# Kernel optimization log

Hardware: AMD Instinct MI355X
Metric: run time of the kernel (lower is better)

## Reference

```python
import jax, jax.numpy as jnp
import numpy as np

B, N, S, K, D = 16, 4096, 1024, 32, 64
MLP = (64, 64, 128)
EPS = 1e-5  # BatchNorm2d default eps


def setup_inputs() -> dict:
    key = jax.random.key(0)
    ks = jax.random.split(key, 16)
    inp = {
        'xyz': jax.random.normal(ks[0], (B, N, 3), dtype=jnp.float32),
        'normals': jax.random.normal(ks[1], (B, N, 3), dtype=jnp.float32),
        'points': jax.random.normal(ks[2], (B, N, D), dtype=jnp.float32),
        'fps_idx': jax.random.randint(ks[3], (B, S), 0, N),
    }
    last = D
    for i, c in enumerate(MLP):
        inp[f'w{i}'] = jax.random.normal(ks[4 + i], (c, last), dtype=jnp.float32) * (1.0 / np.sqrt(last))
        inp[f'b{i}'] = jnp.zeros((c,), dtype=jnp.float32)
        inp[f'g{i}'] = jnp.ones((c,), dtype=jnp.float32)
        inp[f'bt{i}'] = jnp.zeros((c,), dtype=jnp.float32)
        last = c
    return inp


def _group(points, idx):
    # points: [B,N,C], idx: [B,S,K] -> [B,S,K,C]
    b, s, k = idx.shape
    flat = idx.reshape(b, s * k)
    g = jnp.take_along_axis(points, flat[:, :, None], axis=1)
    return g.reshape(b, s, k, points.shape[-1])


def _forward(xyz, normals, points, fps_idx, params):
    new_xyz = jnp.take_along_axis(xyz, fps_idx[:, :, None], axis=1)        # [B,S,3]
    new_normals = jnp.take_along_axis(normals, fps_idx[:, :, None], axis=1)
    # squared distances [B,S,N] (algebraic form of the broadcasted cdist)
    d = (jnp.sum(new_xyz ** 2, -1)[:, :, None]
         + jnp.sum(xyz ** 2, -1)[:, None, :]
         - 2.0 * jnp.einsum('bsc,bnc->bsn', new_xyz, xyz))
    _, idx = jax.lax.top_k(-d, K)                                          # K nearest
    x = _group(points, idx)                                                # [B,S,K,D]
    x = jnp.transpose(x, (0, 3, 2, 1))                                     # [B,D,K,S]
    for (w, b, g, bt) in params:
        x = jnp.einsum('oc,bcks->boks', w, x) + b[None, :, None, None]     # 1x1 conv
        m = jnp.mean(x, axis=(0, 2, 3), keepdims=True)                     # BN (batch stats)
        v = jnp.var(x, axis=(0, 2, 3), keepdims=True)
        x = (x - m) * jax.lax.rsqrt(v + EPS) * g[None, :, None, None] + bt[None, :, None, None]
        x = jax.nn.relu(x)
    feat = jnp.transpose(jnp.max(x, axis=2), (0, 2, 1))                    # [B,S,C_out]
    return new_xyz, new_normals, feat, fps_idx


def reference(xyz, normals, points, fps_idx,
              w0, b0, g0, bt0, w1, b1, g1, bt1, w2, b2, g2, bt2):
    params = ((w0, b0, g0, bt0), (w1, b1, g1, bt1), (w2, b2, g2, bt2))
    return _forward(xyz, normals, points, fps_idx, params)
```

## Files before the change

kernel.cpp:

```cpp
#include <hip/hip_runtime.h>
#include <hip/hip_bf16.h>

#define B_ 16
#define N_ 4096
#define S_ 1024
#define K_ 32
#define D_ 64
#define M_ (B_*S_*K_)
#define EPS_ 1e-5f

#define OUT_NRM  (B_*S_*3)
#define OUT_FEAT (2*B_*S_*3)
#define OUT_FPS  (OUT_FEAT + B_*S_*128)

typedef __attribute__((ext_vector_type(8))) short bf16x8;
typedef __attribute__((ext_vector_type(4))) float f32x4;
typedef unsigned long long u64;

__device__ __forceinline__ unsigned short rnb(float x){
  return (unsigned short)((__float_as_uint(x) + 0x8000u) >> 16);
}
__device__ __forceinline__ void split1(float x, short& h, short& l){
  unsigned ux = __float_as_uint(x);
  unsigned uh = (ux + 0x8000u) & 0xFFFF0000u;
  h = (short)(uh >> 16);
  float lo = x - __uint_as_float(uh);
  l = (short)((__float_as_uint(lo) + 0x8000u) >> 16);
}
__device__ __forceinline__ unsigned f2key(float d){
  unsigned u = __float_as_uint(d);
  return u ^ ((unsigned)(((int)u) >> 31) | 0x80000000u);
}
__device__ __forceinline__ unsigned mprefix(u64 m){
  return __builtin_amdgcn_mbcnt_hi((unsigned)(m >> 32),
         __builtin_amdgcn_mbcnt_lo((unsigned)m, 0u));
}

__device__ __forceinline__ float hred4_sum(const float v[4], int l){
  bool hi8 = (l & 8) != 0;
  float send0 = hi8 ? v[0] : v[2];
  float send1 = hi8 ? v[1] : v[3];
  float r0 = __shfl_xor(send0, 8);
  float r1 = __shfl_xor(send1, 8);
  float a0 = (hi8 ? v[2] : v[0]) + r0;
  float a1 = (hi8 ? v[3] : v[1]) + r1;
  bool hi4 = (l & 4) != 0;
  float send = hi4 ? a0 : a1;
  float r = __shfl_xor(send, 4);
  float a = (hi4 ? a1 : a0) + r;
  a += __shfl_xor(a, 2);
  a += __shfl_xor(a, 1);
  return a;
}
__device__ __forceinline__ float hred4_max(const float v[4], int l){
  bool hi8 = (l & 8) != 0;
  float send0 = hi8 ? v[0] : v[2];
  float send1 = hi8 ? v[1] : v[3];
  float r0 = __shfl_xor(send0, 8);
  float r1 = __shfl_xor(send1, 8);
  float a0 = fmaxf(hi8 ? v[2] : v[0], r0);
  float a1 = fmaxf(hi8 ? v[3] : v[1], r1);
  bool hi4 = (l & 4) != 0;
  float send = hi4 ? a0 : a1;
  float r = __shfl_xor(send, 4);
  float a = fmaxf(hi4 ? a1 : a0, r);
  a = fmaxf(a, __shfl_xor(a, 2));
  a = fmaxf(a, __shfl_xor(a, 1));
  return a;
}

__device__ __forceinline__ void bsort64_f32x2(float& v0, float& v1, int l){
  #pragma unroll
  for (int k = 2; k <= 64; k <<= 1){
    #pragma unroll
    for (int j = k >> 1; j > 0; j >>= 1){
      bool keepmn = (((l & k) == 0) == ((l & j) == 0));
      float o0 = __shfl_xor(v0, j);
      float o1 = __shfl_xor(v1, j);
      v0 = keepmn ? fminf(v0, o0) : fmaxf(v0, o0);
      v1 = keepmn ? fminf(v1, o1) : fmaxf(v1, o1);
    }
  }
}
__device__ __forceinline__ void bsort64_u64x2(u64& v0, u64& v1, int l){
  #pragma unroll
  for (int k = 2; k <= 64; k <<= 1){
    #pragma unroll
    for (int j = k >> 1; j > 0; j >>= 1){
      bool keepmn = (((l & k) == 0) == ((l & j) == 0));
      u64 o0 = __shfl_xor((unsigned long long)v0, j);
      u64 o1 = __shfl_xor((unsigned long long)v1, j);
      bool a0 = v0 < o0, a1 = v1 < o1;
      v0 = (a0 == keepmn) ? v0 : o0;
      v1 = (a1 == keepmn) ? v1 : o1;
    }
  }
}

__global__ void prep_kernel(const float* __restrict__ xyz, const float* __restrict__ nrm,
                            const int* __restrict__ fps,
                            const float* __restrict__ w0, const float* __restrict__ w1,
                            const float* __restrict__ w2,
                            float* __restrict__ out, float4* __restrict__ px,
                            unsigned short* __restrict__ wdst, float* __restrict__ stats){
  const int bid = blockIdx.x, tid = threadIdx.x;
  if (bid < 256){
    int t = bid*256 + tid;
    const float* p = xyz + (size_t)t*3;
    float x = p[0], y = p[1], z = p[2];
    float pp = __fadd_rn(__fadd_rn(__fmul_rn(x,x), __fmul_rn(y,y)), __fmul_rn(z,z));
    px[t] = make_float4(__fmul_rn(-2.f,x), __fmul_rn(-2.f,y), __fmul_rn(-2.f,z), pp);
  } else if (bid < 320){
    int t = (bid-256)*256 + tid;
    int b = t >> 10;
    int n = fps[t];
    const float* xp = xyz + ((size_t)b*N_ + n)*3;
    out[t*3+0] = xp[0]; out[t*3+1] = xp[1]; out[t*3+2] = xp[2];
    const float* pp = nrm + ((size_t)b*N_ + n)*3;
    out[OUT_NRM + t*3+0] = pp[0]; out[OUT_NRM + t*3+1] = pp[1]; out[OUT_NRM + t*3+2] = pp[2];
    out[OUT_FPS + t] = (float)n;
  } else if (bid < 384){
    int e = (bid-320)*256 + tid;
    const float* W; int base;
    if (e < 4096){ W = w0; base = 0; }
    else if (e < 8192){ W = w1; base = 4096; }
    else { W = w2; base = 8192; }
    int r = e - base;
    int frag = r >> 9;
    int lane = (r >> 3) & 63;
    int j = r & 7;
    int cht = frag >> 1, ks = frag & 1;
    int m = lane & 15, quad = lane >> 4;
    int ch = cht*16 + m, k = ks*32 + quad*8 + j;
    wdst[e] = rnb(W[ch*64 + k]);
  } else {
    stats[(bid-384)*256 + tid] = 0.f;
  }
}

#define DISTA(P,QX,QY,QZ,QQ) __builtin_fmaf((P).x,(QX), \
  __builtin_fmaf((P).y,(QY), __builtin_fmaf((P).z,(QZ), (P).w + (QQ))))

__device__ __forceinline__ float dist_exact(float4 P, float qx, float qy, float qz, float qq){
  float px = -0.5f*P.x, py = -0.5f*P.y, pz = -0.5f*P.z;
  float dt = __fadd_rn(__fadd_rn(__fmul_rn(qx,px), __fmul_rn(qy,py)), __fmul_rn(qz,pz));
  return __fsub_rn(__fadd_rn(qq,P.w), __fmul_rn(2.f,dt));
}

#define MARGIN_ 1e-3f

__device__ __forceinline__ void sel_fallback(const u64* sp, unsigned tot, int l,
                                             int* __restrict__ outp){
  if (tot <= 64){
    u64 pair = sp[l];
    u64 plo = 0, phi = (1ull << 44) - 1;
    for (int it = 0; it < 44; ++it){
      u64 mid = plo + ((phi - plo) >> 1);
      u64 m = __ballot(pair <= mid);
      if (__popcll(m) >= 32) phi = mid; else plo = mid + 1;
    }
    bool sel = (pair <= plo);
    u64 m = __ballot(sel);
    unsigned pos = mprefix(m);
    if (sel) outp[pos] = (int)(pair & 0xFFFull);
  } else {
    u64 pa = sp[l], pb = sp[64 + l];
    u64 plo = 0, phi = (1ull << 44) - 1;
    for (int it = 0; it < 44; ++it){
      u64 mid = plo + ((phi - plo) >> 1);
      int c = __popcll(__ballot(pa <= mid)) + __popcll(__ballot(pb <= mid));
      if (c >= 32) phi = mid; else plo = mid + 1;
    }
    int ca = (pa <= plo) ? 1 : 0;
    int cb = (pb <= plo) ? 1 : 0;
    int c2 = ca + cb, inc = c2;
    #pragma unroll
    for (int off = 1; off < 64; off <<= 1){
      int tv = __shfl_up(inc, off);
      if (l >= off) inc += tv;
    }
    int pos = inc - c2;
    if (ca){ outp[pos] = (int)(pa & 0xFFFull); pos++; }
    if (cb){ outp[pos] = (int)(pb & 0xFFFull); }
  }
}

__global__ __launch_bounds__(256, 8) void knn_kernel(const float4* __restrict__ pxyz,
                                                     const int* __restrict__ fps,
                                                     int* __restrict__ idxout){
  __shared__ u64 spair[4][2][128];
  const int t = threadIdx.x, w = t >> 6, l = t & 63;
  const int b = blockIdx.x >> 7;
  const float4* __restrict__ Pp = pxyz + (size_t)b*N_;
  const int q0 = blockIdx.x*8 + w*2;
  const int nq0 = fps[q0], nq1 = fps[q0+1];
  const float4 Q0 = Pp[nq0], Q1 = Pp[nq1];
  const float qx0 = -0.5f*Q0.x, qy0 = -0.5f*Q0.y, qz0 = -0.5f*Q0.z, qq0 = Q0.w;
  const float qx1 = -0.5f*Q1.x, qy1 = -0.5f*Q1.y, qz1 = -0.5f*Q1.z, qq1 = Q1.w;

  float vmin0 = 3.0e38f, vmin1 = 3.0e38f;
  #pragma unroll 8
  for (int i = 0; i < 64; i++){
    float4 P = Pp[i*64 + l];
    float d0 = DISTA(P, qx0, qy0, qz0, qq0); vmin0 = fminf(vmin0, d0);
    float d1 = DISTA(P, qx1, qy1, qz1, qq1); vmin1 = fminf(vmin1, d1);
  }

  float s0 = vmin0, s1 = vmin1;
  bsort64_f32x2(s0, s1, l);
  const float Tm0 = __shfl(s0, 31) + MARGIN_;
  const float Tm1 = __shfl(s1, 31) + MARGIN_;

  spair[w][0][l] = ~0ull; spair[w][0][64 + l] = ~0ull;
  spair[w][1][l] = ~0ull; spair[w][1][64 + l] = ~0ull;

  unsigned cnt0 = 0, cnt1 = 0;
  #pragma unroll 4
  for (int i = 0; i < 64; i++){
    unsigned n = (unsigned)(i*64 + l);
    float4 P = Pp[n];
    {
      float da = DISTA(P, qx0, qy0, qz0, qq0);
      bool c = (da <= Tm0);
      u64 m = __ballot(c);
      if (c){
        float de = dist_exact(P, qx0, qy0, qz0, qq0);
        unsigned pos = cnt0 + mprefix(m);
        if (pos < 128) spair[w][0][pos] = ((u64)f2key(de) << 12) | n;
      }
      cnt0 += (unsigned)__popcll(m);
    }
    {
      float da = DISTA(P, qx1, qy1, qz1, qq1);
      bool c = (da <= Tm1);
      u64 m = __ballot(c);
      if (c){
        float de = dist_exact(P, qx1, qy1, qz1, qq1);
        unsigned pos = cnt1 + mprefix(m);
        if (pos < 128) spair[w][1][pos] = ((u64)f2key(de) << 12) | n;
      }
      cnt1 += (unsigned)__popcll(m);
    }
  }

  const size_t obase = (size_t)q0 * K_;
  if (cnt0 <= 64 && cnt1 <= 64){
    u64 P0 = spair[w][0][l], P1 = spair[w][1][l];
    bsort64_u64x2(P0, P1, l);
    if (l < 32){
      idxout[obase + l]      = (int)(P0 & 0xFFFull);
      idxout[obase + K_ + l] = (int)(P1 & 0xFFFull);
    }
  } else {
    sel_fallback(&spair[w][0][0], cnt0, l, idxout + obase);
    sel_fallback(&spair[w][1][0], cnt1, l, idxout + obase + K_);
  }
}

__global__ __launch_bounds__(256, 4) void conv1_mfma(const float* __restrict__ pts,
    const int* __restrict__ idx, const unsigned short* __restrict__ wpk,
    const float* __restrict__ bias, unsigned short* __restrict__ Yo,
    float* __restrict__ stats){
  __shared__ float sred[4][128];
  __shared__ uint4 Wl4[512];
  const unsigned short* Wl = (const unsigned short*)Wl4;
  const int t = threadIdx.x, w = t>>6, l = t&63, quad = l>>4, lr = l&15;
  const int m0 = blockIdx.x*128;
  const int Rw = m0 + w*32;
  const int b = m0 >> 15;
  Wl4[t] = ((const uint4*)wpk)[t];
  Wl4[256 + t] = ((const uint4*)wpk)[256 + t];
  f32x4 acc[4][2];
  #pragma unroll
  for (int c = 0; c < 4; c++)
    #pragma unroll
    for (int rt = 0; rt < 2; rt++)
      acc[c][rt] = (f32x4){0.f,0.f,0.f,0.f};
  int ri[2];
  #pragma unroll
  for (int rt = 0; rt < 2; rt++) ri[rt] = idx[Rw + rt*16 + lr];
  __syncthreads();
  #pragma unroll
  for (int s = 0; s < 2; s++){
    bf16x8 wfs[4];
    #pragma unroll
    for (int c = 0; c < 4; c++)
      wfs[c] = *(const bf16x8*)(Wl + (((c*2+s)<<6) + l)*8);
    #pragma unroll
    for (int rt = 0; rt < 2; rt++){
      const float* pr = pts + ((size_t)(b*4096 + ri[rt]))*64;
      float4 v0 = *(const float4*)(pr + s*32 + quad*8);
      float4 v1 = *(const float4*)(pr + s*32 + quad*8 + 4);
      float xs[8] = {v0.x,v0.y,v0.z,v0.w,v1.x,v1.y,v1.z,v1.w};
      bf16x8 xh, xl;
      #pragma unroll
      for (int j = 0; j < 8; j++){ short hh, ll; split1(xs[j], hh, ll); xh[j]=hh; xl[j]=ll; }
      #pragma unroll
      for (int c = 0; c < 4; c++){
        acc[c][rt] = __builtin_amdgcn_mfma_f32_16x16x32_bf16(wfs[c], xh, acc[c][rt], 0,0,0);
        acc[c][rt] = __builtin_amdgcn_mfma_f32_16x16x32_bf16(wfs[c], xl, acc[c][rt], 0,0,0);
      }
    }
  }
  const int rtg0 = Rw >> 4;
  #pragma unroll
  for (int c = 0; c < 4; c++){
    float4 bq = *(const float4*)(bias + c*16 + quad*4);
    float bqa[4] = {bq.x, bq.y, bq.z, bq.w};
    float sv[4] = {0,0,0,0}, qv[4] = {0,0,0,0};
    int kb = c*2 + (quad>>1);
    int sub = (quad&1)*4;
    #pragma unroll
    for (int rt = 0; rt < 2; rt++){
      float y[4];
      #pragma unroll
      for (int r = 0; r < 4; r++){
        y[r] = acc[c][rt][r] + bqa[r];
        sv[r] += y[r];
        qv[r] += y[r]*y[r];
      }
      uint2 p;
      p.x = (unsigned)rnb(y[0]) | ((unsigned)rnb(y[1])<<16);
      p.y = (unsigned)rnb(y[2]) | ((unsigned)rnb(y[3])<<16);
      *(uint2*)(Yo + ((((rtg0+rt)*8 + kb)*16 + lr)*8 + sub)) = p;
    }
    float S = hred4_sum(sv, l);
    float Q = hred4_sum(qv, l);
    if ((l & 3) == 0){
      int ch = c*16 + quad*4 + ((l>>3)&1)*2 + ((l>>2)&1);
      sred[w][ch] = S;
      sred[w][64 + ch] = Q;
    }
  }
  __syncthreads();
  if (t < 128){
    float tot = sred[0][t]+sred[1][t]+sred[2][t]+sred[3][t];
    unsafeAtomicAdd(&stats[(blockIdx.x & 7)*512 + t], tot);
  }
}

__global__ __launch_bounds__(256, 4) void conv2_mfma(const unsigned short* __restrict__ Yi,
    const unsigned short* __restrict__ wpk, const float* __restrict__ bias,
    const float* __restrict__ gg, const float* __restrict__ btv,
    unsigned short* __restrict__ Yo, float* __restrict__ stats){
  __shared__ float sred[4][128];
  __shared__ float sAff[128];
  __shared__ uint4 Wl4[512];
  const unsigned short* Wl = (const unsigned short*)Wl4;
  const int t = threadIdx.x, w = t>>6, l = t&63, quad = l>>4, lr = l&15;
  const int m0 = blockIdx.x*128;
  const int Rw = m0 + w*32;
  Wl4[t] = ((const uint4*)wpk)[t];
  Wl4[256 + t] = ((const uint4*)wpk)[256 + t];
  if (t < 64){
    const float inv = 1.f/(float)M_;
    float S = 0.f, Q = 0.f;
    #pragma unroll
    for (int r = 0; r < 8; r++){
      S += stats[r*512 + t];
      Q += stats[r*512 + 64 + t];
    }
    float mean = S * inv;
    float var  = Q * inv - mean*mean;
    float a = gg[t] * rsqrtf(var + EPS_);
    sAff[t] = a;
    sAff[64 + t] = btv[t] - mean*a;
  }
  f32x4 acc[4][2];
  #pragma unroll
  for (int c = 0; c < 4; c++)
    #pragma unroll
    for (int rt = 0; rt < 2; rt++)
      acc[c][rt] = (f32x4){0.f,0.f,0.f,0.f};
  const int rtg0 = Rw >> 4;
  uint4 u[2][2];
  #pragma unroll
  for (int s = 0; s < 2; s++)
    #pragma unroll
    for (int rt = 0; rt < 2; rt++)
      u[s][rt] = *(const uint4*)(Yi + (((rtg0+rt)*8 + s*4 + quad)*16 + lr)*8);
  __syncthreads();
  #pragma unroll
  for (int s = 0; s < 2; s++){
    float4 A0 = *(const float4*)(sAff + s*32 + quad*8);
    float4 A1 = *(const float4*)(sAff + s*32 + quad*8 + 4);
    float4 B0 = *(const float4*)(sAff + 64 + s*32 + quad*8);
    float4 B1 = *(const float4*)(sAff + 64 + s*32 + quad*8 + 4);
    float aA[8] = {A0.x,A0.y,A0.z,A0.w,A1.x,A1.y,A1.z,A1.w};
    float aB[8] = {B0.x,B0.y,B0.z,B0.w,B1.x,B1.y,B1.z,B1.w};
    bf16x8 wfs[4];
    #pragma unroll
    for (int c = 0; c < 4; c++)
      wfs[c] = *(const bf16x8*)(Wl + (((c*2+s)<<6) + l)*8);
    #pragma unroll
    for (int rt = 0; rt < 2; rt++){
      unsigned ua[4] = {u[s][rt].x, u[s][rt].y, u[s][rt].z, u[s][rt].w};
      bf16x8 xb;
      #pragma unroll
      for (int j = 0; j < 8; j++){
        unsigned wd = ua[j>>1];
        float yf = __uint_as_float((j&1) ? (wd & 0xFFFF0000u) : (wd << 16));
        float x = fmaxf(0.f, fmaf(yf, aA[j], aB[j]));
        xb[j] = (short)rnb(x);
      }
      #pragma unroll
      for (int c = 0; c < 4; c++)
        acc[c][rt] = __builtin_amdgcn_mfma_f32_16x16x32_bf16(wfs[c], xb, acc[c][rt], 0,0,0);
    }
  }
  #pragma unroll
  for (int c = 0; c < 4; c++){
    float4 bq = *(const float4*)(bias + c*16 + quad*4);
    float bqa[4] = {bq.x, bq.y, bq.z, bq.w};
    float sv[4] = {0,0,0,0}, qv[4] = {0,0,0,0};
    int kb = c*2 + (quad>>1);
    int sub = (quad&1)*4;
    #pragma unroll
    for (int rt = 0; rt < 2; rt++){
      float y[4];
      #pragma unroll
      for (int r = 0; r < 4; r++){
        y[r] = acc[c][rt][r] + bqa[r];
        sv[r] += y[r];
        qv[r] += y[r]*y[r];
      }
      uint2 p;
      p.x = (unsigned)rnb(y[0]) | ((unsigned)rnb(y[1])<<16);
      p.y = (unsigned)rnb(y[2]) | ((unsigned)rnb(y[3])<<16);
      *(uint2*)(Yo + ((((rtg0+rt)*8 + kb)*16 + lr)*8 + sub)) = p;
    }
    float S = hred4_sum(sv, l);
    float Q = hred4_sum(qv, l);
    if ((l & 3) == 0){
      int ch = c*16 + quad*4 + ((l>>3)&1)*2 + ((l>>2)&1);
      sred[w][ch] = S;
      sred[w][64 + ch] = Q;
    }
  }
  __syncthreads();
  if (t < 128){
    float tot = sred[0][t]+sred[1][t]+sred[2][t]+sred[3][t];
    unsafeAtomicAdd(&stats[(blockIdx.x & 7)*512 + 128 + t], tot);
  }
}

__global__ __launch_bounds__(256, 3) void conv3_mfma(const unsigned short* __restrict__ Yi,
    const unsigned short* __restrict__ wpk, const float* __restrict__ bias,
    const float* __restrict__ gg, const float* __restrict__ btv,
    float* __restrict__ ymax, float* __restrict__ stats){
  __shared__ float sred[4][256];
  __shared__ float sAff[128];
  __shared__ uint4 Wl4[1024];
  const unsigned short* Wl = (const unsigned short*)Wl4;
  const int t = threadIdx.x, w = t>>6, l = t&63, quad = l>>4, lr = l&15;
  const int m0 = blockIdx.x*128;
  const int Rw = m0 + w*32;
  #pragma unroll
  for (int i = 0; i < 4; i++) Wl4[i*256 + t] = ((const uint4*)wpk)[i*256 + t];
  if (t < 64){
    const float inv = 1.f/(float)M_;
    float S = 0.f, Q = 0.f;
    #pragma unroll
    for (int r = 0; r < 8; r++){
      S += stats[r*512 + 128 + t];
      Q += stats[r*512 + 192 + t];
    }
    float mean = S * inv;
    float var  = Q * inv - mean*mean;
    float a = gg[t] * rsqrtf(var + EPS_);
    sAff[t] = a;
    sAff[64 + t] = btv[t] - mean*a;
  }
  f32x4 acc[8][2];
  #pragma unroll
  for (int c = 0; c < 8; c++){
    acc[c][0] = (f32x4){0.f,0.f,0.f,0.f};
    acc[c][1] = (f32x4){0.f,0.f,0.f,0.f};
  }
  const int rtg0 = Rw >> 4;
  uint4 u[2][2];
  #pragma unroll
  for (int s = 0; s < 2; s++)
    #pragma unroll
    for (int rt = 0; rt < 2; rt++)
      u[s][rt] = *(const uint4*)(Yi + (((rtg0+rt)*8 + s*4 + quad)*16 + lr)*8);
  __syncthreads();
  #pragma unroll
  for (int s = 0; s < 2; s++){
    float4 A0 = *(const float4*)(sAff + s*32 + quad*8);
    float4 A1 = *(const float4*)(sAff + s*32 + quad*8 + 4);
    float4 B0 = *(const float4*)(sAff + 64 + s*32 + quad*8);
    float4 B1 = *(const float4*)(sAff + 64 + s*32 + quad*8 + 4);
    float aA[8] = {A0.x,A0.y,A0.z,A0.w,A1.x,A1.y,A1.z,A1.w};
    float aB[8] = {B0.x,B0.y,B0.z,B0.w,B1.x,B1.y,B1.z,B1.w};
    #pragma unroll
    for (int rt = 0; rt < 2; rt++){
      unsigned ua[4] = {u[s][rt].x, u[s][rt].y, u[s][rt].z, u[s][rt].w};
      bf16x8 xb;
      #pragma unroll
      for (int j = 0; j < 8; j++){
        unsigned wd = ua[j>>1];
        float yf = __uint_as_float((j&1) ? (wd & 0xFFFF0000u) : (wd << 16));
        float x = fmaxf(0.f, fmaf(yf, aA[j], aB[j]));
        xb[j] = (short)rnb(x);
      }
      #pragma unroll
      for (int c = 0; c < 8; c++){
        bf16x8 wfc = *(const bf16x8*)(Wl + (((c*2+s)<<6) + l)*8);
        acc[c][rt] = __builtin_amdgcn_mfma_f32_16x16x32_bf16(wfc, xb, acc[c][rt], 0,0,0);
      }
    }
  }
  const int g = Rw >> 5;
  #pragma unroll
  for (int c = 0; c < 8; c++){
    float4 bq = *(const float4*)(bias + c*16 + quad*4);
    float bqa[4] = {bq.x, bq.y, bq.z, bq.w};
    float sv[4], qv[4], mv[4];
    #pragma unroll
    for (int r = 0; r < 4; r++){
      float y0 = acc[c][0][r] + bqa[r];
      float y1 = acc[c][1][r] + bqa[r];
      sv[r] = y0 + y1;
      qv[r] = y0*y0 + y1*y1;
      mv[r] = fmaxf(y0, y1);
    }
    float S = hred4_sum(sv, l);
    float Q = hred4_sum(qv, l);
    float Mx = hred4_max(mv, l);
    if ((l & 3) == 0){
      int ch = c*16 + quad*4 + ((l>>3)&1)*2 + ((l>>2)&1);
      sred[w][ch] = S;
      sred[w][128 + ch] = Q;
      ymax[(size_t)g*128 + ch] = Mx;
    }
  }
  __syncthreads();
  {
    float tot = sred[0][t]+sred[1][t]+sred[2][t]+sred[3][t];
    unsafeAtomicAdd(&stats[(blockIdx.x & 7)*512 + 256 + t], tot);
  }
}

__global__ void final_kernel(const float* __restrict__ ymax,
                             const float* __restrict__ stats,
                             const float* __restrict__ gg, const float* __restrict__ btv,
                             float* __restrict__ out){
  __shared__ float sA[128], sB[128];
  const int tid = threadIdx.x;
  if (tid < 128){
    const float inv = 1.f/(float)M_;
    float S = 0.f, Q = 0.f;
    #pragma unroll
    for (int r = 0; r < 8; r++){
      S += stats[r*512 + 256 + tid];
      Q += stats[r*512 + 384 + tid];
    }
    float mean = S * inv;
    float var  = Q * inv - mean*mean;
    float a = gg[tid] * rsqrtf(var + EPS_);
    sA[tid] = a;
    sB[tid] = btv[tid] - mean*a;
  }
  __syncthreads();
  const size_t base = ((size_t)blockIdx.x*256 + tid)*8;
  float4 v0 = *(const float4*)(ymax + base);
  float4 v1 = *(const float4*)(ymax + base + 4);
  const int c0 = (int)(base & 127);
  float4 a0 = *(const float4*)(sA + c0);
  float4 a1 = *(const float4*)(sA + c0 + 4);
  float4 b0 = *(const float4*)(sB + c0);
  float4 b1 = *(const float4*)(sB + c0 + 4);
  float4 o0, o1;
  o0.x = fmaxf(0.f, a0.x*v0.x + b0.x); o0.y = fmaxf(0.f, a0.y*v0.y + b0.y);
  o0.z = fmaxf(0.f, a0.z*v0.z + b0.z); o0.w = fmaxf(0.f, a0.w*v0.w + b0.w);
  o1.x = fmaxf(0.f, a1.x*v1.x + b1.x); o1.y = fmaxf(0.f, a1.y*v1.y + b1.y);
  o1.z = fmaxf(0.f, a1.z*v1.z + b1.z); o1.w = fmaxf(0.f, a1.w*v1.w + b1.w);
  *(float4*)(out + OUT_FEAT + base) = o0;
  *(float4*)(out + OUT_FEAT + base + 4) = o1;
}

extern "C" void kernel_launch(void* const* d_in, const int* in_sizes, int n_in,
                              void* d_out, int out_size, void* d_ws, size_t ws_size,
                              hipStream_t stream) {
  const float* xyz = (const float*)d_in[0];
  const float* nrm = (const float*)d_in[1];
  const float* pts = (const float*)d_in[2];
  const int*   fps = (const int*)d_in[3];
  const float* w0  = (const float*)d_in[4];
  const float* b0  = (const float*)d_in[5];
  const float* g0  = (const float*)d_in[6];
  const float* bt0 = (const float*)d_in[7];
  const float* w1  = (const float*)d_in[8];
  const float* b1  = (const float*)d_in[9];
  const float* g1  = (const float*)d_in[10];
  const float* bt1 = (const float*)d_in[11];
  const float* w2  = (const float*)d_in[12];
  const float* b2  = (const float*)d_in[13];
  const float* g2  = (const float*)d_in[14];
  const float* bt2 = (const float*)d_in[15];
  float* out = (float*)d_out;

  char* ws = (char*)d_ws;
  float* stats = (float*)ws;
  int*   idxb  = (int*)(ws + 20480);
  float* ymax  = (float*)(ws + 2117632);
  float4* pxyz = (float4*)(ws + 10506240);
  unsigned short* wpack = (unsigned short*)(ws + 11554816);
  unsigned short* Y1 = (unsigned short*)(ws + 18878464);
  unsigned short* Y2 = (unsigned short*)(ws + 85987328);

  prep_kernel<<<400, 256, 0, stream>>>(xyz, nrm, fps, w0, w1, w2, out, pxyz, wpack, stats);
  knn_kernel<<<2048, 256, 0, stream>>>(pxyz, fps, idxb);
  conv1_mfma<<<4096, 256, 0, stream>>>(pts, idxb, wpack, b0, Y1, stats);
  conv2_mfma<<<4096, 256, 0, stream>>>(Y1, wpack + 4096, b1, g0, bt0, Y2, stats);
  conv3_mfma<<<4096, 256, 0, stream>>>(Y2, wpack + 8192, b2, g1, bt1, ymax, stats);
  final_kernel<<<1024, 256, 0, stream>>>(ymax, stats, g2, bt2, out);
}
```

Before: 242.5 us.

## Run MLP on unique points with multiplicity-weighted BN stats, gather-max afterwards

Because the 1x1 conv MLP is pointwise, the three conv layers now run over the B*N source points (65536 rows) instead of the B*S*K grouped rows (524288). A histogram kernel counts how many times each point is selected by kNN, and these counts weight the BatchNorm sums so the batch statistics still match the grouped tensor. A new maxpool kernel gathers the final-layer outputs by neighbor index and takes the max over K. This cuts conv work by 8x, at the cost of an atomic histogram pass, a 32 MB fp32 intermediate and a scattered gather in the pooling step.

```diff
diff --git a/kernel.cpp b/kernel.cpp
--- a/kernel.cpp
+++ b/kernel.cpp
@@ -7,6 +7,7 @@
 #define K_ 32
 #define D_ 64
 #define M_ (B_*S_*K_)
+#define U_ (B_*N_)
 #define EPS_ 1e-5f
 
 #define OUT_NRM  (B_*S_*3)
@@ -52,22 +53,6 @@
   a += __shfl_xor(a, 1);
   return a;
 }
-__device__ __forceinline__ float hred4_max(const float v[4], int l){
-  bool hi8 = (l & 8) != 0;
-  float send0 = hi8 ? v[0] : v[2];
-  float send1 = hi8 ? v[1] : v[3];
-  float r0 = __shfl_xor(send0, 8);
-  float r1 = __shfl_xor(send1, 8);
-  float a0 = fmaxf(hi8 ? v[2] : v[0], r0);
-  float a1 = fmaxf(hi8 ? v[3] : v[1], r1);
-  bool hi4 = (l & 4) != 0;
-  float send = hi4 ? a0 : a1;
-  float r = __shfl_xor(send, 4);
-  float a = fmaxf(hi4 ? a1 : a0, r);
-  a = fmaxf(a, __shfl_xor(a, 2));
-  a = fmaxf(a, __shfl_xor(a, 1));
-  return a;
-}
 
 __device__ __forceinline__ void bsort64_f32x2(float& v0, float& v1, int l){
   #pragma unroll
@@ -102,7 +87,8 @@
                             const float* __restrict__ w0, const float* __restrict__ w1,
                             const float* __restrict__ w2,
                             float* __restrict__ out, float4* __restrict__ px,
-                            unsigned short* __restrict__ wdst, float* __restrict__ stats){
+                            unsigned short* __restrict__ wdst, float* __restrict__ stats,
+                            unsigned* __restrict__ mult){
   const int bid = blockIdx.x, tid = threadIdx.x;
   if (bid < 256){
     int t = bid*256 + tid;
@@ -133,8 +119,10 @@
     int m = lane & 15, quad = lane >> 4;
     int ch = cht*16 + m, k = ks*32 + quad*8 + j;
     wdst[e] = rnb(W[ch*64 + k]);
+  } else if (bid < 400){
+    stats[(bid-384)*256 + tid] = 0.f;
   } else {
-    stats[(bid-384)*256 + tid] = 0.f;
+    mult[(bid-400)*256 + tid] = 0u;
   }
 }
 
@@ -257,17 +245,21 @@
   }
 }
 
+__global__ void hist_kernel(const int* __restrict__ idx, unsigned* __restrict__ mult){
+  int i = blockIdx.x*256 + threadIdx.x;
+  int b = i >> 15;
+  atomicAdd(&mult[b*4096 + idx[i]], 1u);
+}
+
 __global__ __launch_bounds__(256, 4) void conv1_mfma(const float* __restrict__ pts,
-    const int* __restrict__ idx, const unsigned short* __restrict__ wpk,
+    const unsigned* __restrict__ mult, const unsigned short* __restrict__ wpk,
     const float* __restrict__ bias, unsigned short* __restrict__ Yo,
     float* __restrict__ stats){
   __shared__ float sred[4][128];
   __shared__ uint4 Wl4[512];
   const unsigned short* Wl = (const unsigned short*)Wl4;
   const int t = threadIdx.x, w = t>>6, l = t&63, quad = l>>4, lr = l&15;
-  const int m0 = blockIdx.x*128;
-  const int Rw = m0 + w*32;
-  const int b = m0 >> 15;
+  const int Rw = blockIdx.x*128 + w*32;
   Wl4[t] = ((const uint4*)wpk)[t];
   Wl4[256 + t] = ((const uint4*)wpk)[256 + t];
   f32x4 acc[4][2];
@@ -276,9 +268,9 @@
     #pragma unroll
     for (int rt = 0; rt < 2; rt++)
       acc[c][rt] = (f32x4){0.f,0.f,0.f,0.f};
-  int ri[2];
-  #pragma unroll
-  for (int rt = 0; rt < 2; rt++) ri[rt] = idx[Rw + rt*16 + lr];
+  float mf[2];
+  mf[0] = (float)mult[Rw + lr];
+  mf[1] = (float)mult[Rw + 16 + lr];
   __syncthreads();
   #pragma unroll
   for (int s = 0; s < 2; s++){
@@ -288,7 +280,7 @@
       wfs[c] = *(const bf16x8*)(Wl + (((c*2+s)<<6) + l)*8);
     #pragma unroll
     for (int rt = 0; rt < 2; rt++){
-      const float* pr = pts + ((size_t)(b*4096 + ri[rt]))*64;
+      const float* pr = pts + (size_t)(Rw + rt*16 + lr)*64;
       float4 v0 = *(const float4*)(pr + s*32 + quad*8);
       float4 v1 = *(const float4*)(pr + s*32 + quad*8 + 4);
       float xs[8] = {v0.x,v0.y,v0.z,v0.w,v1.x,v1.y,v1.z,v1.w};
@@ -316,8 +308,8 @@
       #pragma unroll
       for (int r = 0; r < 4; r++){
         y[r] = acc[c][rt][r] + bqa[r];
-        sv[r] += y[r];
-        qv[r] += y[r]*y[r];
+        sv[r] += mf[rt]*y[r];
+        qv[r] += mf[rt]*y[r]*y[r];
       }
       uint2 p;
       p.x = (unsigned)rnb(y[0]) | ((unsigned)rnb(y[1])<<16);
@@ -340,16 +332,16 @@
 }
 
 __global__ __launch_bounds__(256, 4) void conv2_mfma(const unsigned short* __restrict__ Yi,
-    const unsigned short* __restrict__ wpk, const float* __restrict__ bias,
-    const float* __restrict__ gg, const float* __restrict__ btv,
-    unsigned short* __restrict__ Yo, float* __restrict__ stats){
+    const unsigned* __restrict__ mult, const unsigned short* __restrict__ wpk,
+    const float* __restrict__ bias, const float* __restrict__ gg,
+    const float* __restrict__ btv, unsigned short* __restrict__ Yo,
+    float* __restrict__ stats){
   __shared__ float sred[4][128];
   __shared__ float sAff[128];
   __shared__ uint4 Wl4[512];
   const unsigned short* Wl = (const unsigned short*)Wl4;
   const int t = threadIdx.x, w = t>>6, l = t&63, quad = l>>4, lr = l&15;
-  const int m0 = blockIdx.x*128;
-  const int Rw = m0 + w*32;
+  const int Rw = blockIdx.x*128 + w*32;
   Wl4[t] = ((const uint4*)wpk)[t];
   Wl4[256 + t] = ((const uint4*)wpk)[256 + t];
   if (t < 64){
@@ -372,6 +364,9 @@
     #pragma unroll
     for (int rt = 0; rt < 2; rt++)
       acc[c][rt] = (f32x4){0.f,0.f,0.f,0.f};
+  float mf[2];
+  mf[0] = (float)mult[Rw + lr];
+  mf[1] = (float)mult[Rw + 16 + lr];
   const int rtg0 = Rw >> 4;
   uint4 u[2][2];
   #pragma unroll
@@ -421,8 +416,8 @@
       #pragma unroll
       for (int r = 0; r < 4; r++){
         y[r] = acc[c][rt][r] + bqa[r];
-        sv[r] += y[r];
-        qv[r] += y[r]*y[r];
+        sv[r] += mf[rt]*y[r];
+        qv[r] += mf[rt]*y[r]*y[r];
       }
       uint2 p;
       p.x = (unsigned)rnb(y[0]) | ((unsigned)rnb(y[1])<<16);
@@ -445,16 +440,16 @@
 }
 
 __global__ __launch_bounds__(256, 3) void conv3_mfma(const unsigned short* __restrict__ Yi,
-    const unsigned short* __restrict__ wpk, const float* __restrict__ bias,
-    const float* __restrict__ gg, const float* __restrict__ btv,
-    float* __restrict__ ymax, float* __restrict__ stats){
+    const unsigned* __restrict__ mult, const unsigned short* __restrict__ wpk,
+    const float* __restrict__ bias, const float* __restrict__ gg,
+    const float* __restrict__ btv, float* __restrict__ zout,
+    float* __restrict__ stats){
   __shared__ float sred[4][256];
   __shared__ float sAff[128];
   __shared__ uint4 Wl4[1024];
   const unsigned short* Wl = (const unsigned short*)Wl4;
   const int t = threadIdx.x, w = t>>6, l = t&63, quad = l>>4, lr = l&15;
-  const int m0 = blockIdx.x*128;
-  const int Rw = m0 + w*32;
+  const int Rw = blockIdx.x*128 + w*32;
   #pragma unroll
   for (int i = 0; i < 4; i++) Wl4[i*256 + t] = ((const uint4*)wpk)[i*256 + t];
   if (t < 64){
@@ -477,6 +472,9 @@
     acc[c][0] = (f32x4){0.f,0.f,0.f,0.f};
     acc[c][1] = (f32x4){0.f,0.f,0.f,0.f};
   }
+  float mf[2];
+  mf[0] = (float)mult[Rw + lr];
+  mf[1] = (float)mult[Rw + 16 + lr];
   const int rtg0 = Rw >> 4;
   uint4 u[2][2];
   #pragma unroll
@@ -511,28 +509,30 @@
       }
     }
   }
-  const int g = Rw >> 5;
   #pragma unroll
   for (int c = 0; c < 8; c++){
     float4 bq = *(const float4*)(bias + c*16 + quad*4);
     float bqa[4] = {bq.x, bq.y, bq.z, bq.w};
-    float sv[4], qv[4], mv[4];
-    #pragma unroll
-    for (int r = 0; r < 4; r++){
-      float y0 = acc[c][0][r] + bqa[r];
-      float y1 = acc[c][1][r] + bqa[r];
-      sv[r] = y0 + y1;
-      qv[r] = y0*y0 + y1*y1;
-      mv[r] = fmaxf(y0, y1);
+    float sv[4], qv[4];
+    #pragma unroll
+    for (int rt = 0; rt < 2; rt++){
+      float y[4];
+      #pragma unroll
+      for (int r = 0; r < 4; r++){
+        y[r] = acc[c][rt][r] + bqa[r];
+        float wy = mf[rt]*y[r];
+        if (rt == 0){ sv[r] = wy; qv[r] = wy*y[r]; }
+        else        { sv[r] += wy; qv[r] += wy*y[r]; }
+      }
+      *(float4*)(zout + (size_t)(Rw + rt*16 + lr)*128 + c*16 + quad*4)
+          = make_float4(y[0], y[1], y[2], y[3]);
     }
     float S = hred4_sum(sv, l);
     float Q = hred4_sum(qv, l);
-    float Mx = hred4_max(mv, l);
     if ((l & 3) == 0){
       int ch = c*16 + quad*4 + ((l>>3)&1)*2 + ((l>>2)&1);
       sred[w][ch] = S;
       sred[w][128 + ch] = Q;
-      ymax[(size_t)g*128 + ch] = Mx;
     }
   }
   __syncthreads();
@@ -540,6 +540,26 @@
     float tot = sred[0][t]+sred[1][t]+sred[2][t]+sred[3][t];
     unsafeAtomicAdd(&stats[(blockIdx.x & 7)*512 + 256 + t], tot);
   }
+}
+
+__global__ __launch_bounds__(256, 8) void maxpool_kernel(const int* __restrict__ idx,
+    const float* __restrict__ zout, float* __restrict__ ymax){
+  __shared__ int sid[4][32];
+  const int t = threadIdx.x, w = t>>6, l = t&63;
+  const int q = blockIdx.x*4 + w;
+  if (l < 32) sid[w][l] = idx[q*32 + l];
+  __syncthreads();
+  const float* zb = zout + (size_t)(q >> 10) * 4096 * 128;
+  float mx = -3.4e38f, my = -3.4e38f;
+  #pragma unroll 8
+  for (int s = 0; s < 32; s++){
+    const float* zp = zb + (size_t)sid[w][s]*128 + l*2;
+    float vx = zp[0], vy = zp[1];
+    mx = fmaxf(mx, vx);
+    my = fmaxf(my, vy);
+  }
+  ymax[(size_t)q*128 + l*2]     = mx;
+  ymax[(size_t)q*128 + l*2 + 1] = my;
 }
 
 __global__ void final_kernel(const float* __restrict__ ymax,
@@ -607,13 +627,17 @@
   float* ymax  = (float*)(ws + 2117632);
   float4* pxyz = (float4*)(ws + 10506240);
   unsigned short* wpack = (unsigned short*)(ws + 11554816);
-  unsigned short* Y1 = (unsigned short*)(ws + 18878464);
-  unsigned short* Y2 = (unsigned short*)(ws + 85987328);
-
-  prep_kernel<<<400, 256, 0, stream>>>(xyz, nrm, fps, w0, w1, w2, out, pxyz, wpack, stats);
+  unsigned* mult = (unsigned*)(ws + 11620352);
+  unsigned short* Y1 = (unsigned short*)(ws + 16777216);
+  unsigned short* Y2 = (unsigned short*)(ws + 33554432);
+  float* zout = (float*)(ws + 50331648);
+
+  prep_kernel<<<656, 256, 0, stream>>>(xyz, nrm, fps, w0, w1, w2, out, pxyz, wpack, stats, mult);
   knn_kernel<<<2048, 256, 0, stream>>>(pxyz, fps, idxb);
-  conv1_mfma<<<4096, 256, 0, stream>>>(pts, idxb, wpack, b0, Y1, stats);
-  conv2_mfma<<<4096, 256, 0, stream>>>(Y1, wpack + 4096, b1, g0, bt0, Y2, stats);
-  conv3_mfma<<<4096, 256, 0, stream>>>(Y2, wpack + 8192, b2, g1, bt1, ymax, stats);
+  hist_kernel<<<2048, 256, 0, stream>>>(idxb, mult);
+  conv1_mfma<<<512, 256, 0, stream>>>(pts, mult, wpack, b0, Y1, stats);
+  conv2_mfma<<<512, 256, 0, stream>>>(Y1, mult, wpack + 4096, b1, g0, bt0, Y2, stats);
+  conv3_mfma<<<512, 256, 0, stream>>>(Y2, mult, wpack + 8192, b2, g1, bt1, zout, stats);
+  maxpool_kernel<<<4096, 256, 0, stream>>>(idxb, zout, ymax);
   final_kernel<<<1024, 256, 0, stream>>>(ymax, stats, g2, bt2, out);
 }
```

New measurement: 217.2 us. -10.4%, faster.
